# Performance work log

Measured on AMD Instinct MI355X. Metric: run time of the kernel, lower is better.

The kernel has to match this reference:

```python
import jax, jax.numpy as jnp
import numpy as np

D_H = 128
BATCH = 131072


def setup_inputs() -> dict:
    key = jax.random.key(0)
    k_h, k_x, k_w = jax.random.split(key, 3)
    h = jax.random.normal(k_h, (BATCH, D_H), dtype=jnp.float32)
    x = jax.random.normal(k_x, (BATCH, 3 * D_H), dtype=jnp.float32)
    # Dense kernel (d_h, 3*d_h); original uses zeros init, but random weights
    # give a meaningful correctness baseline.
    W = jax.random.normal(k_w, (D_H, 3 * D_H), dtype=jnp.float32) * 0.05
    return {"h": h, "x": x, "W": W}


def reference(h, x, W):
    d_h = h.shape[-1]
    # recurrent_proj(h): (B, d_h) @ (d_h, 3*d_h) -> (B, 3*d_h)
    recurrent_t = jnp.einsum("bd,de->be", h, W)
    # input pre-activation uses first d_h slice; gates use remaining 2*d_h
    input_t = jnp.tanh(x[:, :d_h] + recurrent_t[:, :d_h])
    gates_t = jax.nn.sigmoid(x[:, d_h:] + recurrent_t[:, d_h:])
    input_gate_t, output_gate_t = jnp.split(gates_t, 2, axis=-1)
    forget_gate_t = 1.0 - input_gate_t  # tied gates
    h_new = input_t * input_gate_t + h * forget_gate_t
    y = jnp.tanh(h_new) * output_gate_t
    return (h_new, y)
```

## Files before the change

### kernel.cpp

```cpp
#include <hip/hip_runtime.h>
#include <hip/hip_bf16.h>

#define BATCH 131072
#define DH 128
#define D3 384

typedef float   f32x4  __attribute__((ext_vector_type(4)));
typedef __bf16  bf16x8 __attribute__((ext_vector_type(8)));
typedef unsigned short u16x8 __attribute__((ext_vector_type(8)));

__device__ __forceinline__ unsigned short f2bf(float f) {
    unsigned u = __builtin_bit_cast(unsigned, f);
    u += 0x7fffu + ((u >> 16) & 1u);
    return (unsigned short)(u >> 16);
}
__device__ __forceinline__ float fast_tanh(float v) {
    float e = __expf(2.0f * v);
    return (e - 1.0f) * __builtin_amdgcn_rcpf(e + 1.0f);
}
__device__ __forceinline__ float fast_sigmoid(float z) {
    return __builtin_amdgcn_rcpf(1.0f + __expf(-z));
}

__global__ void prep_kernel(const float* __restrict__ W, unsigned short* __restrict__ wt) {
    const int k = blockIdx.x;
    const int e = threadIdx.x;
    wt[e * DH + k] = f2bf(W[k * D3 + e]);
}

__global__ __launch_bounds__(256) void fused_kernel(
    const float* __restrict__ h, const float* __restrict__ x,
    const unsigned short* __restrict__ wt, float* __restrict__ out)
{
    const int wave = (blockIdx.x * 256 + (int)threadIdx.x) >> 6;
    const int lane = threadIdx.x & 63;
    const int c    = lane & 15;
    const int g    = lane >> 4;
    const int tile = wave >> 1;
    const int q    = wave & 1;
    const int row  = tile * 16 + c;
    const int dbase = 64 * q + 4 * g;

    const float* xr = x + (size_t)row * D3;
    const float* hr = h + (size_t)row * DH;

    f32x4 acc[3][4];
    #pragma unroll
    for (int grp = 0; grp < 3; ++grp) {
        #pragma unroll
        for (int n = 0; n < 4; ++n) {
            const f32x4* p = reinterpret_cast<const f32x4*>(xr + grp * DH + dbase + 16 * n);
            acc[grp][n] = __builtin_nontemporal_load(p);
        }
    }

    bf16x8 b[4];
    #pragma unroll
    for (int s = 0; s < 4; ++s) {
        const float4* p = reinterpret_cast<const float4*>(hr + 32 * s + 8 * g);
        float4 u0 = p[0], u1 = p[1];
        u16x8 t;
        t[0]=f2bf(u0.x); t[1]=f2bf(u0.y); t[2]=f2bf(u0.z); t[3]=f2bf(u0.w);
        t[4]=f2bf(u1.x); t[5]=f2bf(u1.y); t[6]=f2bf(u1.z); t[7]=f2bf(u1.w);
        b[s] = __builtin_bit_cast(bf16x8, t);
    }

    #pragma unroll
    for (int grp = 0; grp < 3; ++grp) {
        #pragma unroll
        for (int n = 0; n < 4; ++n) {
            const int ebase = grp * DH + 64 * q + 16 * n;
            const u16x8* wp = reinterpret_cast<const u16x8*>(wt + (size_t)(ebase + c) * DH);
            #pragma unroll
            for (int s = 0; s < 4; ++s) {
                acc[grp][n] = __builtin_amdgcn_mfma_f32_16x16x32_bf16(
                    __builtin_bit_cast(bf16x8, wp[4 * s + g]), b[s], acc[grp][n], 0, 0, 0);
            }
        }
    }

    float* o0 = out + (size_t)row * DH;
    float* o1 = out + (size_t)BATCH * DH + (size_t)row * DH;
    #pragma unroll
    for (int n = 0; n < 4; ++n) {
        const int d = dbase + 16 * n;
        f32x4 hv = *reinterpret_cast<const f32x4*>(hr + d);
        f32x4 v0, v1;
        #pragma unroll
        for (int j = 0; j < 4; ++j) {
            float it = fast_tanh(acc[0][n][j]);
            float ig = fast_sigmoid(acc[1][n][j]);
            float og = fast_sigmoid(acc[2][n][j]);
            float hn = it * ig + hv[j] * (1.0f - ig);
            v0[j] = hn;
            v1[j] = fast_tanh(hn) * og;
        }
        __builtin_nontemporal_store(v0, reinterpret_cast<f32x4*>(o0 + d));
        __builtin_nontemporal_store(v1, reinterpret_cast<f32x4*>(o1 + d));
    }
}

extern "C" void kernel_launch(void* const* d_in, const int* in_sizes, int n_in,
                              void* d_out, int out_size, void* d_ws, size_t ws_size,
                              hipStream_t stream) {
    const float* h = (const float*)d_in[0];
    const float* x = (const float*)d_in[1];
    const float* W = (const float*)d_in[2];
    float* out = (float*)d_out;
    unsigned short* wt = (unsigned short*)d_ws;

    prep_kernel<<<DH, D3, 0, stream>>>(W, wt);
    fused_kernel<<<BATCH / 16 * 2 / 4, 256, 0, stream>>>(h, x, wt, out);
}
```

Measured before the change: 442.5 us.

## Stage per-block weight half in swizzled LDS and share across four waves

Each block now handles 64 rows and one column half, and loads its 192x128 bf16 weight slice into XOR-swizzled shared memory once. The four waves then read MFMA A operands from LDS instead of each issuing its own global loads for the weights. Nontemporal hints on the x loads and output stores are dropped, and launch bounds request 3 blocks per CU. The 48KB LDS per block limits occupancy and adds a barrier plus staging cost to every block.

```diff
diff --git a/kernel.cpp b/kernel.cpp
--- a/kernel.cpp
+++ b/kernel.cpp
@@ -28,53 +28,78 @@
     wt[e * DH + k] = f2bf(W[k * D3 + e]);
 }
 
-__global__ __launch_bounds__(256) void fused_kernel(
+__global__ __launch_bounds__(256, 3) void fused_kernel(
     const float* __restrict__ h, const float* __restrict__ x,
     const unsigned short* __restrict__ wt, float* __restrict__ out)
 {
-    const int wave = (blockIdx.x * 256 + (int)threadIdx.x) >> 6;
-    const int lane = threadIdx.x & 63;
+    __shared__ unsigned char wlds[192 * 256];
+
+    const int tid  = threadIdx.x;
+    const int w    = tid >> 6;
+    const int lane = tid & 63;
     const int c    = lane & 15;
     const int g    = lane >> 4;
-    const int tile = wave >> 1;
-    const int q    = wave & 1;
-    const int row  = tile * 16 + c;
+    const int q    = blockIdx.x & 1;
+    const int RB   = (blockIdx.x >> 1) * 64;
+    const int row  = RB + 16 * w + c;
     const int dbase = 64 * q + 4 * g;
 
+    u16x8 sv[12];
+    #pragma unroll
+    for (int it = 0; it < 12; ++it) {
+        const int i = tid + 256 * it;
+        const int l = i >> 4;
+        const int e = (l >> 6) * 128 + 64 * q + (l & 63);
+        sv[it] = *reinterpret_cast<const u16x8*>(wt + e * DH + (i & 15) * 8);
+    }
+
     const float* xr = x + (size_t)row * D3;
-    const float* hr = h + (size_t)row * DH;
-
     f32x4 acc[3][4];
     #pragma unroll
-    for (int grp = 0; grp < 3; ++grp) {
+    for (int grp = 0; grp < 3; ++grp)
         #pragma unroll
-        for (int n = 0; n < 4; ++n) {
-            const f32x4* p = reinterpret_cast<const f32x4*>(xr + grp * DH + dbase + 16 * n);
-            acc[grp][n] = __builtin_nontemporal_load(p);
-        }
+        for (int n = 0; n < 4; ++n)
+            acc[grp][n] = *reinterpret_cast<const f32x4*>(xr + grp * DH + dbase + 16 * n);
+
+    const float* hr = h + (size_t)row * DH;
+    f32x4 ht[8];
+    #pragma unroll
+    for (int s = 0; s < 4; ++s) {
+        const f32x4* p = reinterpret_cast<const f32x4*>(hr + 32 * s + 8 * g);
+        ht[2 * s]     = p[0];
+        ht[2 * s + 1] = p[1];
     }
 
-    bf16x8 b[4];
+    #pragma unroll
+    for (int it = 0; it < 12; ++it) {
+        const int i  = tid + 256 * it;
+        const int l  = i >> 4;
+        const int bo = ((i & 15) * 16) ^ ((l & 7) << 4);
+        *reinterpret_cast<u16x8*>(&wlds[l * 256 + bo]) = sv[it];
+    }
+
+    bf16x8 bfr[4];
     #pragma unroll
     for (int s = 0; s < 4; ++s) {
-        const float4* p = reinterpret_cast<const float4*>(hr + 32 * s + 8 * g);
-        float4 u0 = p[0], u1 = p[1];
         u16x8 t;
-        t[0]=f2bf(u0.x); t[1]=f2bf(u0.y); t[2]=f2bf(u0.z); t[3]=f2bf(u0.w);
-        t[4]=f2bf(u1.x); t[5]=f2bf(u1.y); t[6]=f2bf(u1.z); t[7]=f2bf(u1.w);
-        b[s] = __builtin_bit_cast(bf16x8, t);
+        #pragma unroll
+        for (int j = 0; j < 4; ++j) { t[j] = f2bf(ht[2*s][j]); t[4+j] = f2bf(ht[2*s+1][j]); }
+        bfr[s] = __builtin_bit_cast(bf16x8, t);
     }
+
+    __syncthreads();
 
     #pragma unroll
     for (int grp = 0; grp < 3; ++grp) {
         #pragma unroll
         for (int n = 0; n < 4; ++n) {
-            const int ebase = grp * DH + 64 * q + 16 * n;
-            const u16x8* wp = reinterpret_cast<const u16x8*>(wt + (size_t)(ebase + c) * DH);
+            const unsigned char* base = &wlds[(grp * 64 + 16 * n + c) * 256];
+            const int sw = (c & 7) << 4;
             #pragma unroll
             for (int s = 0; s < 4; ++s) {
+                u16x8 av = *reinterpret_cast<const u16x8*>(base + ((64 * s + 16 * g) ^ sw));
                 acc[grp][n] = __builtin_amdgcn_mfma_f32_16x16x32_bf16(
-                    __builtin_bit_cast(bf16x8, wp[4 * s + g]), b[s], acc[grp][n], 0, 0, 0);
+                    __builtin_bit_cast(bf16x8, av), bfr[s], acc[grp][n], 0, 0, 0);
             }
         }
     }
@@ -95,8 +120,8 @@
             v0[j] = hn;
             v1[j] = fast_tanh(hn) * og;
         }
-        __builtin_nontemporal_store(v0, reinterpret_cast<f32x4*>(o0 + d));
-        __builtin_nontemporal_store(v1, reinterpret_cast<f32x4*>(o1 + d));
+        *reinterpret_cast<f32x4*>(o0 + d) = v0;
+        *reinterpret_cast<f32x4*>(o1 + d) = v1;
     }
 }
 
@@ -110,5 +135,5 @@
     unsigned short* wt = (unsigned short*)d_ws;
 
     prep_kernel<<<DH, D3, 0, stream>>>(W, wt);
-    fused_kernel<<<BATCH / 16 * 2 / 4, 256, 0, stream>>>(h, x, wt, out);
+    fused_kernel<<<(BATCH / 64) * 2, 256, 0, stream>>>(h, x, wt, out);
 }
```

After: 365.4 us. -17.4%, faster.
